# Performance work log

Measured on AMD Instinct MI355X. Metric: run time of the kernel, lower is better.

Reference implementation:

```python
import jax, jax.numpy as jnp
import numpy as np

M1 = 32
M2 = 32
S1 = 64
S2 = 64
TWO_PI = jnp.float32(2.0 * np.pi)


def setup_inputs() -> dict:
    key = jax.random.key(0)
    k1, k2, k3, k4, k5 = jax.random.split(key, 5)
    B, C, N = 8, 64, 16384
    x = jax.random.normal(k1, (B, C, N), dtype=jnp.float32)
    x_in = jax.random.uniform(k2, (B, N, 2), dtype=jnp.float32)
    x_out = jax.random.uniform(k3, (B, N, 2), dtype=jnp.float32)
    # xavier_normal for fan_in=64, fan_out=64 over [i,o,m,2]
    std = jnp.float32(np.sqrt(2.0 / (64 + 64)))
    w1 = std * jax.random.normal(k4, (64, 64, M2, 2), dtype=jnp.float32)
    w2 = std * jax.random.normal(k5, (64, 64, M1, 2), dtype=jnp.float32)
    return {"x": x, "x_in": x_in, "x_out": x_out, "w1": w1, "w2": w2}


def reference(x, x_in, x_out, w1, w2):
    # iphi = identity: mapped coords are the mesh coords themselves.
    # Original code repeats the 1-D NUFFT bases along the grid dims (s1/s2)
    # before the einsums; since the repeated axis is constant, the final
    # contraction over it is exactly a factor s1 (resp. s2). We compute the
    # mathematically identical form without materializing [B,N,m,s] tensors.
    Wy = w1[..., 0] + 1j * w1[..., 1]  # [i, o, m2] complex
    Wx = w2[..., 0] + 1j * w2[..., 1]  # [i, o, m1] complex
    ky = jnp.arange(M2, dtype=jnp.float32)
    kx = jnp.arange(M1, dtype=jnp.float32)

    # forward NUFFT bases from x_in  (exp(-i 2 pi k . p))
    bfy = jnp.exp(-1j * TWO_PI * x_in[..., 0:1] * ky)   # [B, N, m2]
    bfx = jnp.exp(-1j * TWO_PI * x_in[..., 1:2] * kx)   # [B, N, m1]
    # inverse NUFFT bases from x_out (exp(+i 2 pi k . p))
    ibfy = jnp.exp(1j * TWO_PI * x_out[..., 0:1] * ky)  # [B, N, m2]
    ibfx = jnp.exp(1j * TWO_PI * x_out[..., 1:2] * kx)  # [B, N, m1]

    xc = x.astype(jnp.complex64)

    # y-direction branch (fourier_weight[0])
    fty = jnp.einsum('bcn,bny->bcy', xc, bfy)           # [B, in, m2]
    my = jnp.einsum('biy,ioy->boy', fty, Wy)            # [B, out, m2]
    xy = S1 * jnp.einsum('boy,bny->bon', my, ibfy).real  # [B, out, N]

    # x-direction branch (fourier_weight[1])
    ftx = jnp.einsum('bcn,bnx->bcx', xc, bfx)           # [B, in, m1]
    mx = jnp.einsum('bix,iox->box', ftx, Wx)            # [B, out, m1]
    xx = S2 * jnp.einsum('box,bnx->bon', mx, ibfx).real  # [B, out, N]

    return xx + xy
```

## Files before the change

### kernel.cpp

```cpp
#include <hip/hip_runtime.h>

#define BB 8
#define CC 64
#define OO 64
#define NN 16384
#define MMODE 32
#define JJ 128
#define SFAC 64.0f

constexpr float TWO_PI_F = 6.28318530717958647692f;

typedef __attribute__((ext_vector_type(8))) short short8;
typedef __attribute__((ext_vector_type(4))) float f32x4;

static __device__ __forceinline__ unsigned short f2bf(float f) {
  unsigned u = __float_as_uint(f);
  u += 0x7FFF + ((u >> 16) & 1);
  return (unsigned short)(u >> 16);
}
static __device__ __forceinline__ unsigned pack2(float a, float b) {
  return (unsigned)f2bf(a) | ((unsigned)f2bf(b) << 16);
}


__global__ __launch_bounds__(256) void fwd_kernel(
    const float* __restrict__ x, const float* __restrict__ x_in,
    float* __restrict__ ft) {
  __shared__ __attribute__((aligned(16))) short bas[JJ * 72];
  __shared__ __attribute__((aligned(16))) short xs[32 * 72];
  __shared__ __attribute__((aligned(16))) float ps[1024];
  const int t = threadIdx.x;
  const int b = blockIdx.z, chalf = blockIdx.y;
  const int n0 = blockIdx.x * 512;

  {
    const float4 v = *(const float4*)&x_in[((size_t)b * NN + n0) * 2 + t * 4];
    *(float4*)&ps[t * 4] = v;
  }
  const int xc = t >> 3, xng = t & 7;
  const float* xbase = x + ((size_t)(b * CC + chalf * 32 + xc)) * NN + n0 + xng * 4;
  float4 ra = *(const float4*)(xbase);
  float4 rb = *(const float4*)(xbase + 32);

  const int w = t >> 6, L = t & 63;
  const int q4 = L >> 4, l15 = L & 15;
  f32x4 acc[4];
#pragma unroll
  for (int i = 0; i < 4; ++i) acc[i] = (f32x4){0.f, 0.f, 0.f, 0.f};

  __syncthreads();

  for (int s = 0; s < 8; ++s) {
    *(uint2*)&xs[xc * 72 + xng * 4]      = make_uint2(pack2(ra.x, ra.y), pack2(ra.z, ra.w));
    *(uint2*)&xs[xc * 72 + xng * 4 + 32] = make_uint2(pack2(rb.x, rb.y), pack2(rb.z, rb.w));
    if (s < 7) {
      ra = *(const float4*)(xbase + (s + 1) * 64);
      rb = *(const float4*)(xbase + (s + 1) * 64 + 32);
    }
#pragma unroll
    for (int ti = 0; ti < 2; ++ti) {
      const int tau = t + ti * 256;
      const int ng = tau & 7, mm = tau >> 3;
      const int br = mm >> 5, m = mm & 31;
      const float fm = -TWO_PI_F * (float)m;
      union { unsigned short u[8]; uint4 v; } R, I;
#pragma unroll
      for (int k = 0; k < 8; ++k) {
        const float p = ps[(s * 64 + ng * 8 + k) * 2 + br];
        float sv, cv;
        __sincosf(fm * p, &sv, &cv);
        R.u[k] = f2bf(cv);
        I.u[k] = f2bf(sv);
      }
      const int row = br * 64 + 2 * m;
      *(uint4*)&bas[row * 72 + ng * 8]       = R.v;
      *(uint4*)&bas[(row + 1) * 72 + ng * 8] = I.v;
    }
    __syncthreads();
#pragma unroll
    for (int ks = 0; ks < 2; ++ks) {
      const int ko = ks * 32 + q4 * 8;
      const short8 a0 = *(const short8*)&bas[(w * 32 + l15) * 72 + ko];
      const short8 a1 = *(const short8*)&bas[(w * 32 + 16 + l15) * 72 + ko];
      const short8 b0 = *(const short8*)&xs[l15 * 72 + ko];
      const short8 b1 = *(const short8*)&xs[(16 + l15) * 72 + ko];
      acc[0] = __builtin_amdgcn_mfma_f32_16x16x32_bf16(a0, b0, acc[0], 0, 0, 0);
      acc[1] = __builtin_amdgcn_mfma_f32_16x16x32_bf16(a0, b1, acc[1], 0, 0, 0);
      acc[2] = __builtin_amdgcn_mfma_f32_16x16x32_bf16(a1, b0, acc[2], 0, 0, 0);
      acc[3] = __builtin_amdgcn_mfma_f32_16x16x32_bf16(a1, b1, acc[3], 0, 0, 0);
    }
    __syncthreads();
  }
  const int jb0 = w * 32 + q4 * 4;
  const int cb = chalf * 32 + l15;
#pragma unroll
  for (int ji = 0; ji < 2; ++ji)
#pragma unroll
    for (int ci = 0; ci < 2; ++ci) {
      const f32x4 v = acc[ji * 2 + ci];
#pragma unroll
      for (int r = 0; r < 4; ++r)
        atomicAdd(&ft[((size_t)b * JJ + jb0 + ji * 16 + r) * CC + cb + ci * 16], v[r]);
    }
}

__global__ __launch_bounds__(64) void mix_kernel(
    const float* __restrict__ ft, const float* __restrict__ w1,
    const float* __restrict__ w2, float* __restrict__ A) {
  __shared__ float fre[64], fim[64];
  const int m = blockIdx.x, branch = blockIdx.y, b = blockIdx.z;
  const int o = threadIdx.x;
  const int jb = branch * 64 + 2 * m;
  fre[o] = ft[((size_t)b * JJ + jb) * CC + o];
  fim[o] = ft[((size_t)b * JJ + jb + 1) * CC + o];
  __syncthreads();
  const float* w = branch ? w2 : w1;
  float ar = 0.f, ai = 0.f;
#pragma unroll 4
  for (int i = 0; i < 64; ++i) {
    const float wr = w[(((size_t)i * 64 + o) * MMODE + m) * 2 + 0];
    const float wi = w[(((size_t)i * 64 + o) * MMODE + m) * 2 + 1];
    ar += fre[i] * wr - fim[i] * wi;
    ai += fre[i] * wi + fim[i] * wr;
  }
  A[((size_t)b * OO + o) * JJ + jb]     =  SFAC * ar;
  A[((size_t)b * OO + o) * JJ + jb + 1] = -SFAC * ai;
}

__global__ __launch_bounds__(256) void inv_kernel(
    const float* __restrict__ x_out, const float* __restrict__ A,
    float* __restrict__ out) {
  __shared__ __attribute__((aligned(16))) short As_s[OO * 136];
  __shared__ __attribute__((aligned(16))) short basn[64 * 136];
  __shared__ __attribute__((aligned(16))) float psI[512];
  const int t = threadIdx.x;
  const int b = blockIdx.y;
  const int n0 = blockIdx.x * 256;

  if (t < 128) {
    const float4 v = *(const float4*)&x_out[((size_t)b * NN + n0) * 2 + t * 4];
    *(float4*)&psI[t * 4] = v;
  }
#pragma unroll
  for (int idx = t; idx < 2048; idx += 256) {
    const int o = idx >> 5, j4 = idx & 31;
    const float4 v = *(const float4*)&A[((size_t)b * OO + o) * JJ + j4 * 4];
    *(uint2*)&As_s[o * 136 + j4 * 4] = make_uint2(pack2(v.x, v.y), pack2(v.z, v.w));
  }
  const int w = t >> 6, L = t & 63;
  const int q4 = L >> 4, l15 = L & 15;
  const int nl = t & 63, q = t >> 6, br = q >> 1, half = q & 1;
  const int ot0 = (w & 1) * 32;
  const int nt0 = (w >> 1) * 32;
  __syncthreads();

  for (int s = 0; s < 4; ++s) {
    {
      const float p = psI[(s * 64 + nl) * 2 + br];
      float s1, c1;
      __sincosf(TWO_PI_F * p, &s1, &c1);
      float brr = 1.f, bii = 0.f;
      if (half) {
        float r = c1, qq = s1;
#pragma unroll
        for (int k = 0; k < 4; ++k) { const float nr = r*r - qq*qq, ni = 2.f*r*qq; r = nr; qq = ni; }
        brr = r; bii = qq;
      }
      short* bp = &basn[nl * 136 + br * 64 + half * 32];
#pragma unroll
      for (int g = 0; g < 4; ++g) {
        union { unsigned short u[8]; uint4 v; } P;
#pragma unroll
        for (int mi = 0; mi < 4; ++mi) {
          P.u[2 * mi]     = f2bf(brr);
          P.u[2 * mi + 1] = f2bf(bii);
          const float nr = brr * c1 - bii * s1, ni = brr * s1 + bii * c1;
          brr = nr; bii = ni;
        }
        *(uint4*)&bp[g * 8] = P.v;
      }
    }
    __syncthreads();
    f32x4 acc[4];
#pragma unroll
    for (int i = 0; i < 4; ++i) acc[i] = (f32x4){0.f, 0.f, 0.f, 0.f};
#pragma unroll
    for (int ks = 0; ks < 4; ++ks) {
      const int ko = ks * 32 + q4 * 8;
      const short8 a0 = *(const short8*)&As_s[(ot0 + l15) * 136 + ko];
      const short8 a1 = *(const short8*)&As_s[(ot0 + 16 + l15) * 136 + ko];
      const short8 b0 = *(const short8*)&basn[(nt0 + l15) * 136 + ko];
      const short8 b1 = *(const short8*)&basn[(nt0 + 16 + l15) * 136 + ko];
      acc[0] = __builtin_amdgcn_mfma_f32_16x16x32_bf16(a0, b0, acc[0], 0, 0, 0);
      acc[1] = __builtin_amdgcn_mfma_f32_16x16x32_bf16(a0, b1, acc[1], 0, 0, 0);
      acc[2] = __builtin_amdgcn_mfma_f32_16x16x32_bf16(a1, b0, acc[2], 0, 0, 0);
      acc[3] = __builtin_amdgcn_mfma_f32_16x16x32_bf16(a1, b1, acc[3], 0, 0, 0);
    }
    const int nbase = n0 + s * 64 + nt0 + l15;
#pragma unroll
    for (int oi = 0; oi < 2; ++oi)
#pragma unroll
      for (int ni = 0; ni < 2; ++ni) {
        const f32x4 v = acc[oi * 2 + ni];
#pragma unroll
        for (int r = 0; r < 4; ++r)
          out[((size_t)b * OO + ot0 + oi * 16 + q4 * 4 + r) * NN + nbase + ni * 16] = v[r];
      }
    __syncthreads();
  }
}

extern "C" void kernel_launch(void* const* d_in, const int* in_sizes, int n_in,
                              void* d_out, int out_size, void* d_ws, size_t ws_size,
                              hipStream_t stream) {
  const float* x     = (const float*)d_in[0];
  const float* x_in  = (const float*)d_in[1];
  const float* x_out = (const float*)d_in[2];
  const float* w1    = (const float*)d_in[3];
  const float* w2    = (const float*)d_in[4];
  float* out = (float*)d_out;
  float* ft = (float*)d_ws;
  float* A  = ft + (size_t)BB * JJ * CC;

  hipMemsetAsync(ft, 0, (size_t)BB * JJ * CC * sizeof(float), stream);
  fwd_kernel<<<dim3(32, 2, BB), 256, 0, stream>>>(x, x_in, ft);
  mix_kernel<<<dim3(MMODE, 2, BB), 64, 0, stream>>>(ft, w1, w2, A);
  inv_kernel<<<dim3(64, BB), 256, 0, stream>>>(x_out, A, out);
}
```

Before: 121.8 us.

## Replace atomic reductions with per-slice partials; use revolution-based hardware sin/cos

The forward kernel now writes per-slice partial spectra to workspace instead of atomically adding into a zeroed buffer, which removes the memset and atomic contention. The mix kernel grows to 256 threads: it reduces the 32 partials, splits the input-channel contraction across four groups, and reads weights as float2. The basis generation switches from __sincosf on radians to range-reduced fractional revolutions passed to the hardware sin/cos builtins, which saves the multiply and the internal range reduction. The cost is a larger workspace (about 8 MB of partials) and extra reads in the mix stage.

```diff
diff --git a/kernel.cpp b/kernel.cpp
--- a/kernel.cpp
+++ b/kernel.cpp
@@ -8,8 +8,6 @@
 #define JJ 128
 #define SFAC 64.0f
 
-constexpr float TWO_PI_F = 6.28318530717958647692f;
-
 typedef __attribute__((ext_vector_type(8))) short short8;
 typedef __attribute__((ext_vector_type(4))) float f32x4;
 
@@ -21,17 +19,19 @@
 static __device__ __forceinline__ unsigned pack2(float a, float b) {
   return (unsigned)f2bf(a) | ((unsigned)f2bf(b) << 16);
 }
+static __device__ __forceinline__ float sin2pi(float x) { return __builtin_amdgcn_sinf(x); }
+static __device__ __forceinline__ float cos2pi(float x) { return __builtin_amdgcn_cosf(x); }
 
 
 __global__ __launch_bounds__(256) void fwd_kernel(
     const float* __restrict__ x, const float* __restrict__ x_in,
-    float* __restrict__ ft) {
+    float* __restrict__ part) {
   __shared__ __attribute__((aligned(16))) short bas[JJ * 72];
   __shared__ __attribute__((aligned(16))) short xs[32 * 72];
   __shared__ __attribute__((aligned(16))) float ps[1024];
   const int t = threadIdx.x;
-  const int b = blockIdx.z, chalf = blockIdx.y;
-  const int n0 = blockIdx.x * 512;
+  const int b = blockIdx.z, chalf = blockIdx.y, sl = blockIdx.x;
+  const int n0 = sl * 512;
 
   {
     const float4 v = *(const float4*)&x_in[((size_t)b * NN + n0) * 2 + t * 4];
@@ -62,15 +62,15 @@
       const int tau = t + ti * 256;
       const int ng = tau & 7, mm = tau >> 3;
       const int br = mm >> 5, m = mm & 31;
-      const float fm = -TWO_PI_F * (float)m;
+      const float fm = (float)m;
       union { unsigned short u[8]; uint4 v; } R, I;
 #pragma unroll
       for (int k = 0; k < 8; ++k) {
         const float p = ps[(s * 64 + ng * 8 + k) * 2 + br];
-        float sv, cv;
-        __sincosf(fm * p, &sv, &cv);
-        R.u[k] = f2bf(cv);
-        I.u[k] = f2bf(sv);
+        float rev = fm * p;
+        rev -= floorf(rev);
+        R.u[k] = f2bf(cos2pi(rev));
+        I.u[k] = f2bf(-sin2pi(rev));
       }
       const int row = br * 64 + 2 * m;
       *(uint4*)&bas[row * 72 + ng * 8]       = R.v;
@@ -91,6 +91,7 @@
     }
     __syncthreads();
   }
+  float* pp = part + (size_t)(b * 32 + sl) * JJ * CC;
   const int jb0 = w * 32 + q4 * 4;
   const int cb = chalf * 32 + l15;
 #pragma unroll
@@ -100,31 +101,53 @@
       const f32x4 v = acc[ji * 2 + ci];
 #pragma unroll
       for (int r = 0; r < 4; ++r)
-        atomicAdd(&ft[((size_t)b * JJ + jb0 + ji * 16 + r) * CC + cb + ci * 16], v[r]);
-    }
-}
-
-__global__ __launch_bounds__(64) void mix_kernel(
-    const float* __restrict__ ft, const float* __restrict__ w1,
+        pp[(jb0 + ji * 16 + r) * CC + cb + ci * 16] = v[r];
+    }
+}
+
+__global__ __launch_bounds__(256) void mix_kernel(
+    const float* __restrict__ part, const float* __restrict__ w1,
     const float* __restrict__ w2, float* __restrict__ A) {
+  __shared__ float red[8][64];
   __shared__ float fre[64], fim[64];
   const int m = blockIdx.x, branch = blockIdx.y, b = blockIdx.z;
-  const int o = threadIdx.x;
+  const int t = threadIdx.x;
+  const int c = t & 63, g = t >> 6;
   const int jb = branch * 64 + 2 * m;
-  fre[o] = ft[((size_t)b * JJ + jb) * CC + o];
-  fim[o] = ft[((size_t)b * JJ + jb + 1) * CC + o];
+  float pre = 0.f, pim = 0.f;
+#pragma unroll
+  for (int k = 0; k < 8; ++k) {
+    const int sl = g + 4 * k;
+    const float* pp = part + (size_t)(b * 32 + sl) * JJ * CC;
+    pre += pp[jb * CC + c];
+    pim += pp[(jb + 1) * CC + c];
+  }
+  red[g * 2][c] = pre;
+  red[g * 2 + 1][c] = pim;
+  __syncthreads();
+  if (t < 64) {
+    fre[t] = red[0][t] + red[2][t] + red[4][t] + red[6][t];
+    fim[t] = red[1][t] + red[3][t] + red[5][t] + red[7][t];
+  }
   __syncthreads();
   const float* w = branch ? w2 : w1;
+  const int o = c;
   float ar = 0.f, ai = 0.f;
 #pragma unroll 4
-  for (int i = 0; i < 64; ++i) {
-    const float wr = w[(((size_t)i * 64 + o) * MMODE + m) * 2 + 0];
-    const float wi = w[(((size_t)i * 64 + o) * MMODE + m) * 2 + 1];
-    ar += fre[i] * wr - fim[i] * wi;
-    ai += fre[i] * wi + fim[i] * wr;
-  }
-  A[((size_t)b * OO + o) * JJ + jb]     =  SFAC * ar;
-  A[((size_t)b * OO + o) * JJ + jb + 1] = -SFAC * ai;
+  for (int ii = 0; ii < 16; ++ii) {
+    const int i = g * 16 + ii;
+    const float2 wv = *(const float2*)&w[(((size_t)i * 64 + o) * MMODE + m) * 2];
+    ar += fre[i] * wv.x - fim[i] * wv.y;
+    ai += fre[i] * wv.y + fim[i] * wv.x;
+  }
+  red[g * 2][o] = ar;
+  red[g * 2 + 1][o] = ai;
+  __syncthreads();
+  if (t < 64) {
+    const float sr = red[0][t] + red[2][t] + red[4][t] + red[6][t];
+    const float si = red[1][t] + red[3][t] + red[5][t] + red[7][t];
+    *(float2*)&A[((size_t)b * OO + t) * JJ + jb] = make_float2(SFAC * sr, -SFAC * si);
+  }
 }
 
 __global__ __launch_bounds__(256) void inv_kernel(
@@ -157,8 +180,8 @@
   for (int s = 0; s < 4; ++s) {
     {
       const float p = psI[(s * 64 + nl) * 2 + br];
-      float s1, c1;
-      __sincosf(TWO_PI_F * p, &s1, &c1);
+      const float fr = p - floorf(p);
+      const float s1 = sin2pi(fr), c1 = cos2pi(fr);
       float brr = 1.f, bii = 0.f;
       if (half) {
         float r = c1, qq = s1;
@@ -219,11 +242,10 @@
   const float* w1    = (const float*)d_in[3];
   const float* w2    = (const float*)d_in[4];
   float* out = (float*)d_out;
-  float* ft = (float*)d_ws;
-  float* A  = ft + (size_t)BB * JJ * CC;
-
-  hipMemsetAsync(ft, 0, (size_t)BB * JJ * CC * sizeof(float), stream);
-  fwd_kernel<<<dim3(32, 2, BB), 256, 0, stream>>>(x, x_in, ft);
-  mix_kernel<<<dim3(MMODE, 2, BB), 64, 0, stream>>>(ft, w1, w2, A);
+  float* part = (float*)d_ws;
+  float* A = part + (size_t)BB * 32 * JJ * CC;
+
+  fwd_kernel<<<dim3(32, 2, BB), 256, 0, stream>>>(x, x_in, part);
+  mix_kernel<<<dim3(MMODE, 2, BB), 256, 0, stream>>>(part, w1, w2, A);
   inv_kernel<<<dim3(64, BB), 256, 0, stream>>>(x_out, A, out);
 }
```

Measured after the change: 119.5 us. About the same (-1.9%).
